# Performance work log

Measured on AMD Instinct MI355X. Metric: run time of the kernel, lower is better.

The kernel has to match this reference:

```python
import jax, jax.numpy as jnp
import numpy as np

# Module config (init_kwargs)
K_PERIODS = 5
PMAX = 512
MIN_PERIOD_THRESHOLD = 2

B, T, N = 32, 2048, 128


def setup_inputs() -> dict:
    key = jax.random.key(0)
    x = jax.random.normal(key, (B, T, N), dtype=jnp.float32)
    return {"x": x}


def reference(x):
    """Faithful dense/padded JAX version of PeriodicityTransform.forward (mask=None).

    The torch module emits ragged PeriodGroups keyed by (cycles, period).
    Since jit requires static shapes, we return the same per-(series, freq)
    information in padded form:
      tiles   : [BN, K, T]  flattened folded tile (row-major cycle x period),
                 zero-padded past take = cycles*periods
      periods : [BN, K] int32
      cycles  : [BN, K] int32
    tiles[bn,k,:take].reshape(cycles, period) equals the torch tile exactly.
    """
    Bq, Tq, Nq = x.shape
    BN = Bq * Nq
    seqs = jnp.transpose(x, (0, 2, 1)).reshape(BN, Tq)  # [BN, T]

    # --- _topk_freq ---
    spec = jnp.fft.rfft(seqs, axis=-1)                   # [BN, T//2+1]
    mag2 = spec.real ** 2 + spec.imag ** 2
    mag2 = mag2.at[..., 0].set(0.0)                      # kill DC
    k = min(K_PERIODS, mag2.shape[-1] - 1)
    _, kidx = jax.lax.top_k(mag2, k)                     # [BN, K]
    kidx = jnp.maximum(kidx, 1).astype(jnp.int32)

    # --- period / cycle computation (valid_lengths == T, no mask) ---
    lengths = jnp.int32(Tq)
    periods = lengths // kidx                            # [BN, K]
    periods = jnp.minimum(periods, PMAX)
    min_period = min(MIN_PERIOD_THRESHOLD, Tq)
    periods = jnp.maximum(periods, min_period)
    periods = jnp.maximum(periods, 1)
    cycles = jnp.maximum(lengths // periods, 1)          # [BN, K]

    take = cycles * periods                              # [BN, K], <= T
    t = jnp.arange(Tq, dtype=jnp.int32)                  # [T]
    start = Tq - take                                    # [BN, K]
    gather_idx = jnp.clip(start[..., None] + t, 0, Tq - 1)  # [BN, K, T]
    valid = t[None, None, :] < take[..., None]           # [BN, K, T]

    src = jnp.broadcast_to(seqs[:, None, :], (BN, k, Tq))
    tiles = jnp.take_along_axis(src, gather_idx, axis=-1)
    tiles = jnp.where(valid, tiles, jnp.zeros((), dtype=tiles.dtype))
    return tiles, periods, cycles
```

## Files before the change

### kernel.cpp

```cpp
#include <hip/hip_runtime.h>

#define B_ 32
#define T_ 2048
#define N_ 128
#define K_ 5
#define BN_ (B_ * N_)
#define PMAX_ 512
#define MINP_ 2

static constexpr double PI_D = 3.14159265358979323846264338327950288;
static constexpr float  S2_F = 0.70710678118654752440f;

struct cf { float r, i; };

__device__ __forceinline__ void bf_w(cf& u, cf& v, float wr, float wi) {
    const float tr = v.r * wr - v.i * wi;
    const float ti = v.r * wi + v.i * wr;
    v.r = u.r - tr; v.i = u.i - ti;
    u.r += tr;      u.i += ti;
}
__device__ __forceinline__ void bf_1(cf& u, cf& v) {
    const float tr = v.r, ti = v.i;
    v.r = u.r - tr; v.i = u.i - ti;
    u.r += tr;      u.i += ti;
}
__device__ __forceinline__ void bf_mi(cf& u, cf& v) {
    const float tr = v.i, ti = -v.r;
    v.r = u.r - tr; v.i = u.i - ti;
    u.r += tr;      u.i += ti;
}
__device__ __forceinline__ int sw(int i) { return i ^ ((i >> 5) & 31); }

__global__ __launch_bounds__(256) void pt_twiddle(float2* __restrict__ tw) {
    const int m = blockIdx.x * 256 + threadIdx.x;
    if (m < 1024) {
        double s, c;
        sincos(-2.0 * PI_D * (double)m / 2048.0, &s, &c);
        tw[m] = make_float2((float)c, (float)s);
    }
}

__global__ __launch_bounds__(256, 4) void pt_fft_tiles(const float* __restrict__ x,
                                                       float* __restrict__ out,
                                                       const float2* __restrict__ tw) {
    __shared__ float re[2048];
    __shared__ float im[2048];
    __shared__ __align__(16) float seqA[2052];
    __shared__ __align__(16) float seqB[2052];
    __shared__ float wredv[4];
    __shared__ int   wredi[4];
    __shared__ int   sh_take[2][K_];

    const int i0  = blockIdx.x;
    const int q   = ((i0 & 7) << 8) | (i0 >> 3);
    const int bn0 = q * 2;
    const int b   = bn0 >> 7;
    const int n   = bn0 & 127;
    const int tid = threadIdx.x;

    const float* xp = x + (size_t)b * T_ * N_ + n;
    float2 v[8];
#pragma unroll
    for (int m = 0; m < 8; ++m)
        v[m] = *(const float2*)(xp + (size_t)(tid + 256 * m) * N_);
#pragma unroll
    for (int m = 0; m < 8; ++m) {
        const int t = tid + 256 * m;
        seqA[t] = v[m].x;
        seqB[t] = v[m].y;
        const int p = sw((int)(__brev((unsigned)t) >> 21));
        re[p] = v[m].x;
        im[p] = v[m].y;
    }
    __syncthreads();

    {
        const int base = tid * 8;
        cf E[8];
#pragma unroll
        for (int j = 0; j < 8; ++j) { const int p = sw(base + j); E[j].r = re[p]; E[j].i = im[p]; }
        bf_1(E[0], E[1]); bf_1(E[2], E[3]); bf_1(E[4], E[5]); bf_1(E[6], E[7]);
        bf_1(E[0], E[2]); bf_mi(E[1], E[3]); bf_1(E[4], E[6]); bf_mi(E[5], E[7]);
        bf_1(E[0], E[4]); bf_w(E[1], E[5], S2_F, -S2_F);
        bf_mi(E[2], E[6]); bf_w(E[3], E[7], -S2_F, -S2_F);
#pragma unroll
        for (int j = 0; j < 8; ++j) { const int p = sw(base + j); re[p] = E[j].r; im[p] = E[j].i; }
    }
    __syncthreads();

#pragma unroll
    for (int r = 0; r < 2; ++r) {
        const int s    = 4 + 3 * r;
        const int h    = 1 << (s - 1);
        const int bq   = tid & (h - 1);
        const int g    = tid >> (s - 1);
        const int base = g * 8 * h + bq;
        const float2 w1  = tw[bq << (11 - s)];
        const float2 w2a = tw[bq << (10 - s)];
        const float2 w2b = tw[(bq + h) << (10 - s)];
        const float2 w30 = tw[bq << (9 - s)];
        const float2 w31 = tw[(bq + h) << (9 - s)];
        const float2 w32 = tw[(bq + 2 * h) << (9 - s)];
        const float2 w33 = tw[(bq + 3 * h) << (9 - s)];
        cf E[8];
#pragma unroll
        for (int j = 0; j < 8; ++j) { const int p = sw(base + j * h); E[j].r = re[p]; E[j].i = im[p]; }
        bf_w(E[0], E[1], w1.x, w1.y);   bf_w(E[2], E[3], w1.x, w1.y);
        bf_w(E[4], E[5], w1.x, w1.y);   bf_w(E[6], E[7], w1.x, w1.y);
        bf_w(E[0], E[2], w2a.x, w2a.y); bf_w(E[1], E[3], w2b.x, w2b.y);
        bf_w(E[4], E[6], w2a.x, w2a.y); bf_w(E[5], E[7], w2b.x, w2b.y);
        bf_w(E[0], E[4], w30.x, w30.y); bf_w(E[1], E[5], w31.x, w31.y);
        bf_w(E[2], E[6], w32.x, w32.y); bf_w(E[3], E[7], w33.x, w33.y);
#pragma unroll
        for (int j = 0; j < 8; ++j) { const int p = sw(base + j * h); re[p] = E[j].r; im[p] = E[j].i; }
        __syncthreads();
    }

#pragma unroll
    for (int u = 0; u < 2; ++u) {
        const int bb = tid + 256 * u;
        const float2 wA = tw[bb << 1];
        const float2 wB = tw[bb];
        const float2 wC = tw[bb + 512];
        const int p0 = sw(bb), p1 = sw(bb + 512), p2 = sw(bb + 1024), p3 = sw(bb + 1536);
        cf E0 = {re[p0], im[p0]}, E1 = {re[p1], im[p1]};
        cf E2 = {re[p2], im[p2]}, E3 = {re[p3], im[p3]};
        bf_w(E0, E1, wA.x, wA.y); bf_w(E2, E3, wA.x, wA.y);
        bf_w(E0, E2, wB.x, wB.y); bf_w(E1, E3, wC.x, wC.y);
        re[p0] = E0.r; im[p0] = E0.i; re[p1] = E1.r; im[p1] = E1.i;
        re[p2] = E2.r; im[p2] = E2.i; re[p3] = E3.r; im[p3] = E3.i;
    }
    __syncthreads();

    float magsA[4], magsB[4];
#pragma unroll
    for (int m = 0; m < 4; ++m) {
        const int k  = 1 + tid + 256 * m;
        const int nk = 2048 - k;
        const int pk = sw(k), pn = sw(nk);
        const float zr = re[pk], zi = im[pk];
        const float yr = re[pn], yi = im[pn];
        const float ar = zr + yr, ai = zi - yi;
        const float br = zi + yi, bi = yr - zr;
        magsA[m] = ar * ar + ai * ai;
        magsB[m] = br * br + bi * bi;
    }
    __syncthreads();
#pragma unroll
    for (int m = 0; m < 4; ++m) {
        const int pk = sw(1 + tid + 256 * m);
        re[pk] = magsA[m];
        im[pk] = magsB[m];
    }
    __syncthreads();

    const int half = tid >> 7;
    const int lt   = tid & 127;
    const int wid  = tid >> 6;
    float* marr = half ? im : re;
    for (int it = 0; it < K_; ++it) {
        float bestv = -2.0f;
        int   besti = 1 << 30;
#pragma unroll
        for (int m = 0; m < 8; ++m) {
            const int k = 1 + lt + 128 * m;
            const float vv = marr[sw(k)];
            if (vv > bestv || (vv == bestv && k < besti)) { bestv = vv; besti = k; }
        }
#pragma unroll
        for (int off = 32; off > 0; off >>= 1) {
            const float v2 = __shfl_down(bestv, off);
            const int   i2 = __shfl_down(besti, off);
            if (v2 > bestv || (v2 == bestv && i2 < besti)) { bestv = v2; besti = i2; }
        }
        if ((tid & 63) == 0) { wredv[wid] = bestv; wredi[wid] = besti; }
        __syncthreads();
        if (lt == 0) {
            float vb = wredv[2 * half]; int ib = wredi[2 * half];
            const float v1 = wredv[2 * half + 1]; const int i1 = wredi[2 * half + 1];
            if (v1 > vb || (v1 == vb && i1 < ib)) { vb = v1; ib = i1; }
            marr[sw(ib)] = -1.0f;
            int period = T_ / ib;
            if (period > PMAX_) period = PMAX_;
            if (period < MINP_) period = MINP_;
            const int cyc = T_ / period;
            sh_take[half][it] = (period << 16) | (period * cyc);
        }
        __syncthreads();
    }

    const size_t TILES = (size_t)BN_ * K_ * T_;
    if (tid < 2 * K_) {
        const int s2 = tid / K_, k2 = tid % K_;
        const int pk   = sh_take[s2][k2];
        const int per  = pk >> 16;
        const int take = pk & 0xFFFF;
        out[TILES + (size_t)(bn0 + s2) * K_ + k2]                      = (float)per;
        out[TILES + (size_t)BN_ * K_ + (size_t)(bn0 + s2) * K_ + k2]   = (float)(take / per);
    }

    float* rowA = out + (size_t)bn0 * (K_ * T_);
#pragma unroll
    for (int m = 0; m < 20; ++m) {
        const int e  = tid + 256 * m;
        const int s2 = (e >= K_ * (T_ / 4)) ? 1 : 0;
        const int w  = e - s2 * (K_ * (T_ / 4));
        const int k  = w >> 9;
        const int p4 = (w & 511) << 2;
        const int take  = sh_take[s2][k] & 0xFFFF;
        const int start = T_ - take;
        const float4* sq4 = (const float4*)(s2 ? seqB : seqA);
        const int idx = start + p4;
        int a0 = idx >> 2;
        if (a0 > 511) a0 = 511;
        const int sh = idx & 3;
        const float4 lo = sq4[a0];
        const float4 hi = sq4[a0 + 1];
        float r0, r1, r2, r3;
        if (sh == 0)      { r0 = lo.x; r1 = lo.y; r2 = lo.z; r3 = lo.w; }
        else if (sh == 1) { r0 = lo.y; r1 = lo.z; r2 = lo.w; r3 = hi.x; }
        else if (sh == 2) { r0 = lo.z; r1 = lo.w; r2 = hi.x; r3 = hi.y; }
        else              { r0 = lo.w; r1 = hi.x; r2 = hi.y; r3 = hi.z; }
        float4 vv;
        vv.x = (p4 + 0 < take) ? r0 : 0.0f;
        vv.y = (p4 + 1 < take) ? r1 : 0.0f;
        vv.z = (p4 + 2 < take) ? r2 : 0.0f;
        vv.w = (p4 + 3 < take) ? r3 : 0.0f;
        *(float4*)(rowA + (size_t)(s2 * K_ + k) * T_ + p4) = vv;
    }
}

extern "C" void kernel_launch(void* const* d_in, const int* in_sizes, int n_in,
                              void* d_out, int out_size, void* d_ws, size_t ws_size,
                              hipStream_t stream) {
    const float* x = (const float*)d_in[0];
    float* out = (float*)d_out;
    float2* tw = (float2*)d_ws;

    pt_twiddle<<<dim3(4), dim3(256), 0, stream>>>(tw);
    pt_fft_tiles<<<dim3(BN_ / 2), dim3(256), 0, stream>>>(x, out, tw);
}
```

Baseline: 225.7 us.

## Halve LDS by reloading input, single-wave register top-k, nontemporal tile stores

Drops the separate seqA/seqB shared buffers and instead reloads the input from global memory after the FFT, reusing the re/im arrays to hold the time series for the tile gather. This roughly halves LDS per block, and the launch-bounds occupancy hint is raised from 4 to 8 blocks. Top-k now runs in one wave per series with the magnitudes held in registers, which removes the per-iteration block-wide barriers. Tile output writes use nontemporal stores. The cost is a second global read of the input and two idle waves during top-k.

```diff
diff --git a/kernel.cpp b/kernel.cpp
--- a/kernel.cpp
+++ b/kernel.cpp
@@ -11,6 +11,8 @@
 static constexpr double PI_D = 3.14159265358979323846264338327950288;
 static constexpr float  S2_F = 0.70710678118654752440f;
 
+typedef float vf4 __attribute__((ext_vector_type(4)));
+
 struct cf { float r, i; };
 
 __device__ __forceinline__ void bf_w(cf& u, cf& v, float wr, float wi) {
@@ -40,16 +42,12 @@
     }
 }
 
-__global__ __launch_bounds__(256, 4) void pt_fft_tiles(const float* __restrict__ x,
+__global__ __launch_bounds__(256, 8) void pt_fft_tiles(const float* __restrict__ x,
                                                        float* __restrict__ out,
                                                        const float2* __restrict__ tw) {
-    __shared__ float re[2048];
-    __shared__ float im[2048];
-    __shared__ __align__(16) float seqA[2052];
-    __shared__ __align__(16) float seqB[2052];
-    __shared__ float wredv[4];
-    __shared__ int   wredi[4];
-    __shared__ int   sh_take[2][K_];
+    __shared__ __align__(16) float re[2052];
+    __shared__ __align__(16) float im[2052];
+    __shared__ int sh_take[2][K_];
 
     const int i0  = blockIdx.x;
     const int q   = ((i0 & 7) << 8) | (i0 >> 3);
@@ -59,18 +57,18 @@
     const int tid = threadIdx.x;
 
     const float* xp = x + (size_t)b * T_ * N_ + n;
-    float2 v[8];
-#pragma unroll
-    for (int m = 0; m < 8; ++m)
-        v[m] = *(const float2*)(xp + (size_t)(tid + 256 * m) * N_);
-#pragma unroll
-    for (int m = 0; m < 8; ++m) {
-        const int t = tid + 256 * m;
-        seqA[t] = v[m].x;
-        seqB[t] = v[m].y;
-        const int p = sw((int)(__brev((unsigned)t) >> 21));
-        re[p] = v[m].x;
-        im[p] = v[m].y;
+    {
+        float2 v[8];
+#pragma unroll
+        for (int m = 0; m < 8; ++m)
+            v[m] = *(const float2*)(xp + (size_t)(tid + 256 * m) * N_);
+#pragma unroll
+        for (int m = 0; m < 8; ++m) {
+            const int t = tid + 256 * m;
+            const int p = sw((int)(__brev((unsigned)t) >> 21));
+            re[p] = v[m].x;
+            im[p] = v[m].y;
+        }
     }
     __syncthreads();
 
@@ -154,40 +152,46 @@
     }
     __syncthreads();
 
-    const int half = tid >> 7;
-    const int lt   = tid & 127;
+    float2 v2[8];
+#pragma unroll
+    for (int m = 0; m < 8; ++m)
+        v2[m] = *(const float2*)(xp + (size_t)(tid + 256 * m) * N_);
+
     const int wid  = tid >> 6;
-    float* marr = half ? im : re;
-    for (int it = 0; it < K_; ++it) {
-        float bestv = -2.0f;
-        int   besti = 1 << 30;
-#pragma unroll
-        for (int m = 0; m < 8; ++m) {
-            const int k = 1 + lt + 128 * m;
-            const float vv = marr[sw(k)];
-            if (vv > bestv || (vv == bestv && k < besti)) { bestv = vv; besti = k; }
+    const int lane = tid & 63;
+    if (wid < 2) {
+        const float* marr = wid ? im : re;
+        float mv[16];
+#pragma unroll
+        for (int j = 0; j < 16; ++j) mv[j] = marr[sw(1 + lane + 64 * j)];
+        for (int it = 0; it < K_; ++it) {
+            float bestv = -2.0f;
+            int   besti = 1 << 30;
+#pragma unroll
+            for (int j = 0; j < 16; ++j) {
+                const int k = 1 + lane + 64 * j;
+                if (mv[j] > bestv || (mv[j] == bestv && k < besti)) { bestv = mv[j]; besti = k; }
+            }
+#pragma unroll
+            for (int off = 32; off > 0; off >>= 1) {
+                const float v3 = __shfl_down(bestv, off);
+                const int   i3 = __shfl_down(besti, off);
+                if (v3 > bestv || (v3 == bestv && i3 < besti)) { bestv = v3; besti = i3; }
+            }
+            const int win = __shfl(besti, 0);
+#pragma unroll
+            for (int j = 0; j < 16; ++j)
+                if (1 + lane + 64 * j == win) mv[j] = -1.0f;
+            if (lane == 0) {
+                int period = T_ / win;
+                if (period > PMAX_) period = PMAX_;
+                if (period < MINP_) period = MINP_;
+                const int cyc = T_ / period;
+                sh_take[wid][it] = (period << 16) | (period * cyc);
+            }
         }
-#pragma unroll
-        for (int off = 32; off > 0; off >>= 1) {
-            const float v2 = __shfl_down(bestv, off);
-            const int   i2 = __shfl_down(besti, off);
-            if (v2 > bestv || (v2 == bestv && i2 < besti)) { bestv = v2; besti = i2; }
-        }
-        if ((tid & 63) == 0) { wredv[wid] = bestv; wredi[wid] = besti; }
-        __syncthreads();
-        if (lt == 0) {
-            float vb = wredv[2 * half]; int ib = wredi[2 * half];
-            const float v1 = wredv[2 * half + 1]; const int i1 = wredi[2 * half + 1];
-            if (v1 > vb || (v1 == vb && i1 < ib)) { vb = v1; ib = i1; }
-            marr[sw(ib)] = -1.0f;
-            int period = T_ / ib;
-            if (period > PMAX_) period = PMAX_;
-            if (period < MINP_) period = MINP_;
-            const int cyc = T_ / period;
-            sh_take[half][it] = (period << 16) | (period * cyc);
-        }
-        __syncthreads();
-    }
+    }
+    __syncthreads();
 
     const size_t TILES = (size_t)BN_ * K_ * T_;
     if (tid < 2 * K_) {
@@ -199,6 +203,14 @@
         out[TILES + (size_t)BN_ * K_ + (size_t)(bn0 + s2) * K_ + k2]   = (float)(take / per);
     }
 
+#pragma unroll
+    for (int m = 0; m < 8; ++m) {
+        const int t = tid + 256 * m;
+        re[t] = v2[m].x;
+        im[t] = v2[m].y;
+    }
+    __syncthreads();
+
     float* rowA = out + (size_t)bn0 * (K_ * T_);
 #pragma unroll
     for (int m = 0; m < 20; ++m) {
@@ -209,24 +221,24 @@
         const int p4 = (w & 511) << 2;
         const int take  = sh_take[s2][k] & 0xFFFF;
         const int start = T_ - take;
-        const float4* sq4 = (const float4*)(s2 ? seqB : seqA);
+        const vf4* sq4 = (const vf4*)(s2 ? im : re);
         const int idx = start + p4;
         int a0 = idx >> 2;
         if (a0 > 511) a0 = 511;
         const int sh = idx & 3;
-        const float4 lo = sq4[a0];
-        const float4 hi = sq4[a0 + 1];
+        const vf4 lo = sq4[a0];
+        const vf4 hi = sq4[a0 + 1];
         float r0, r1, r2, r3;
         if (sh == 0)      { r0 = lo.x; r1 = lo.y; r2 = lo.z; r3 = lo.w; }
         else if (sh == 1) { r0 = lo.y; r1 = lo.z; r2 = lo.w; r3 = hi.x; }
         else if (sh == 2) { r0 = lo.z; r1 = lo.w; r2 = hi.x; r3 = hi.y; }
         else              { r0 = lo.w; r1 = hi.x; r2 = hi.y; r3 = hi.z; }
-        float4 vv;
+        vf4 vv;
         vv.x = (p4 + 0 < take) ? r0 : 0.0f;
         vv.y = (p4 + 1 < take) ? r1 : 0.0f;
         vv.z = (p4 + 2 < take) ? r2 : 0.0f;
         vv.w = (p4 + 3 < take) ? r3 : 0.0f;
-        *(float4*)(rowA + (size_t)(s2 * K_ + k) * T_ + p4) = vv;
+        __builtin_nontemporal_store(vv, (vf4*)(rowA + (size_t)(s2 * K_ + k) * T_ + p4));
     }
 }
 
```

Result: slower. 237.8 us (+5.3%).
